# Kernel optimization log

Measured on AMD Instinct MI355X. Metric: run time of the kernel, lower is better.

## Reference

```python
import jax, jax.numpy as jnp
import numpy as np

BN_EPS = 1e-5
L2_EPS = 1e-12


def setup_inputs() -> dict:
    key = jax.random.key(0)
    k1, k2, k3 = jax.random.split(key, 3)
    B, N, D, K, G = 32, 2048, 512, 64, 16
    init_sc = 1.0 / np.sqrt(D)
    x = jax.random.normal(k1, (B, N, D), dtype=jnp.float32)
    clusters = init_sc * jax.random.normal(k2, (D, K + G), dtype=jnp.float32)
    clusters2 = init_sc * jax.random.normal(k3, (1, D, K), dtype=jnp.float32)
    bn_gamma = jnp.ones((K + G,), dtype=jnp.float32)
    bn_beta = jnp.zeros((K + G,), dtype=jnp.float32)
    return {"x": x, "clusters": clusters, "clusters2": clusters2,
            "bn_gamma": bn_gamma, "bn_beta": bn_beta}


def reference(x, clusters, clusters2, bn_gamma, bn_beta):
    B, N, D = x.shape
    K = clusters2.shape[-1]
    xf = x.reshape(B * N, D)
    # soft cluster assignment: [B*N, K+G]
    assn = xf @ clusters
    # BatchNorm1d (training-mode batch statistics, biased variance)
    mean = jnp.mean(assn, axis=0)
    var = jnp.var(assn, axis=0)
    assn = (assn - mean) * jax.lax.rsqrt(var + BN_EPS) * bn_gamma + bn_beta
    # softmax over clusters, then drop ghost clusters
    assn = jax.nn.softmax(assn, axis=1)[:, :K].reshape(B, N, K)
    # residual aggregation
    a_sum = jnp.sum(assn, axis=1, keepdims=True)          # [B, 1, K]
    a = a_sum * clusters2                                  # [B, D, K]
    vlad = jnp.einsum("bnk,bnd->bdk", assn, x) - a         # [B, D, K]
    # intra-normalization across feature dim D
    vlad = vlad / jnp.maximum(jnp.linalg.norm(vlad, axis=1, keepdims=True), L2_EPS)
    # flatten and global L2 normalization
    vlad = vlad.reshape(B, D * K)
    vlad = vlad / jnp.maximum(jnp.linalg.norm(vlad, axis=1, keepdims=True), L2_EPS)
    return vlad
```

## Files before the change

kernel.cpp:

```cpp
#include <hip/hip_runtime.h>
#include <hip/hip_bf16.h>
#include <stdint.h>

typedef __attribute__((ext_vector_type(8))) short short8;
typedef __attribute__((ext_vector_type(4))) float f32x4;

__device__ __forceinline__ float b2f(uint16_t u) {
  union { uint32_t i; float f; } v; v.i = ((uint32_t)u) << 16; return v.f;
}
__device__ __forceinline__ uint16_t f2b(float f) {
  uint32_t u = __float_as_uint(f);
  return (uint16_t)((u + 0x7FFFu + ((u >> 16) & 1u)) >> 16);
}
__device__ __forceinline__ uint32_t pk2(uint32_t lo, uint32_t hi) {
  return __builtin_amdgcn_perm(hi + 0x8000u, lo + 0x8000u, 0x07060302u);
}

__global__ void k0_prep(const float* __restrict__ clusters,
                        uint16_t* __restrict__ cB) {
  int gid = blockIdx.x * 256 + threadIdx.x;
  if (gid < 40960) {
    int i = gid & 7, chunk = gid >> 3;
    int lr = chunk & 15, q = (chunk >> 4) & 3, c5 = chunk >> 6;
    int n = c5 % 5, kk = c5 / 5;
    cB[gid] = f2b(clusters[(kk * 32 + q * 8 + i) * 80 + n * 16 + lr]);
  }
}

__global__ __launch_bounds__(256) void k1_gemm1(
    const float* __restrict__ x, const uint16_t* __restrict__ cB,
    float* __restrict__ raw, float* __restrict__ part) {
  __shared__ __align__(16) uint16_t lB[80 * 512];
  const int t = threadIdx.x;
  const int w = t >> 6, lane = t & 63, q = lane >> 4, lr = lane & 15;
  const int rbase = blockIdx.x * 128 + w * 32;

  {
    const uint4* src = (const uint4*)cB;
#pragma unroll 4
    for (int it = 0; it < 20; ++it)
      *(uint4*)&lB[(it * 256 + t) * 8] = src[it * 256 + t];
  }

  f32x4 acc[2][5];
#pragma unroll
  for (int m = 0; m < 2; ++m)
#pragma unroll
    for (int n = 0; n < 5; ++n) acc[m][n] = 0.f;

  const float* xa = x + (size_t)(rbase + lr) * 512 + q * 8;
  __syncthreads();

#pragma unroll 8
  for (int kk = 0; kk < 16; ++kk) {
    short8 a[2], bf[5];
#pragma unroll
    for (int m = 0; m < 2; ++m) {
      uint4 u0 = *(const uint4*)(xa + (size_t)m * 16 * 512 + kk * 32);
      uint4 u1 = *(const uint4*)(xa + (size_t)m * 16 * 512 + kk * 32 + 4);
      union { short8 s; uint32_t u[4]; } av;
      av.u[0] = pk2(u0.x, u0.y); av.u[1] = pk2(u0.z, u0.w);
      av.u[2] = pk2(u1.x, u1.y); av.u[3] = pk2(u1.z, u1.w);
      a[m] = av.s;
    }
#pragma unroll
    for (int n = 0; n < 5; ++n)
      bf[n] = *(const short8*)&lB[(((kk * 5 + n) * 4 + q) * 16 + lr) * 8];
#pragma unroll
    for (int m = 0; m < 2; ++m)
#pragma unroll
      for (int n = 0; n < 5; ++n)
        acc[m][n] = __builtin_amdgcn_mfma_f32_16x16x32_bf16(a[m], bf[n], acc[m][n], 0, 0, 0);
  }
  __syncthreads();

  float sums[5], sqs[5];
#pragma unroll
  for (int n = 0; n < 5; ++n) {
    float s = 0.f, qq = 0.f;
#pragma unroll
    for (int m = 0; m < 2; ++m) {
#pragma unroll
      for (int r = 0; r < 4; ++r) {
        float v = acc[m][n][r];
        s += v; qq += v * v;
        raw[(size_t)(rbase + m * 16 + q * 4 + r) * 80 + n * 16 + lr] = v;
      }
    }
    s += __shfl_xor(s, 16);  s += __shfl_xor(s, 32);
    qq += __shfl_xor(qq, 16); qq += __shfl_xor(qq, 32);
    sums[n] = s; sqs[n] = qq;
  }

  float* sf = (float*)lB;
  if (lane < 16) {
#pragma unroll
    for (int n = 0; n < 5; ++n) {
      sf[w * 160 + n * 16 + lr] = sums[n];
      sf[640 + w * 160 + n * 16 + lr] = sqs[n];
    }
  }
  __syncthreads();
  if (t < 160) {
    float a0 = sf[t] + sf[160 + t] + sf[320 + t] + sf[480 + t];
    float b0 = sf[640 + t] + sf[800 + t] + sf[960 + t] + sf[1120 + t];
    part[(size_t)t * 512 + blockIdx.x] = a0;
    part[(size_t)(160 + t) * 512 + blockIdx.x] = b0;
  }
}

__global__ __launch_bounds__(64) void k2_stats(
    const float* __restrict__ part, const float* __restrict__ gamma,
    const float* __restrict__ beta, float* __restrict__ scsh) {
  int c = blockIdx.x, t = threadIdx.x;
  const float* p1 = part + (size_t)c * 512;
  const float* p2 = part + (size_t)(160 + c) * 512;
  float s1 = 0.f, s2 = 0.f;
#pragma unroll
  for (int p = 0; p < 512; p += 64) { s1 += p1[p + t]; s2 += p2[p + t]; }
#pragma unroll
  for (int o = 1; o < 64; o <<= 1) { s1 += __shfl_xor(s1, o); s2 += __shfl_xor(s2, o); }
  if (t == 0) {
    float mean = s1 * (1.f / 65536.f);
    float var = s2 * (1.f / 65536.f) - mean * mean;
    float sc = rsqrtf(var + 1e-5f) * gamma[c];
    scsh[c] = sc;
    scsh[80 + c] = beta[c] - mean * sc;
  }
}

__global__ __launch_bounds__(256, 2) void k34_fused(
    const float* __restrict__ x, const float* __restrict__ raw_,
    const float* __restrict__ scsh, float* __restrict__ vpart,
    float* __restrict__ apart) {
  __shared__ __align__(16) uint16_t sx[2][256 * 40];
  __shared__ __align__(16) uint16_t sp[2][64 * 40];
  __shared__ float sc[80], sh[80];
  __shared__ float ared[4 * 64];

  const int t = threadIdx.x;
  const int b = blockIdx.x >> 4;
  const int s = (blockIdx.x >> 1) & 7;
  const int dh = blockIdx.x & 1;
  const int w = t >> 6, lane = t & 63, q = lane >> 4, lr = lane & 15;

  const int dd = t;
  const int sg = ((dd >> 2) + (dd >> 4)) & 3;
  const int r_ = t >> 3, cg = t & 7;
  const int kk_ = t & 63, ng = t >> 6;

  if (t < 80) sc[t] = scsh[t];
  else if (t < 160) sh[t - 80] = scsh[t];

  const float* xb = x + ((size_t)b * 2048 + (size_t)s * 256) * 512 + dh * 256;
  const float* rawb = raw_ + ((size_t)b * 2048 + (size_t)s * 256) * 80;

  f32x4 acc[4][4];
#pragma unroll
  for (int m = 0; m < 4; ++m)
#pragma unroll
    for (int j = 0; j < 4; ++j) acc[m][j] = 0.f;

  float xf[32], yf[10];
  float asum = 0.f;

#define XLOAD(c)                                                          \
  {                                                                       \
    const float* xc = xb + (size_t)(c) * 32 * 512 + dd;                   \
    _Pragma("unroll")                                                     \
    for (int j = 0; j < 32; ++j) xf[j] = xc[(size_t)j * 512];             \
  }
#define RLOAD(c)                                                          \
  {                                                                       \
    const float* rc = rawb + (size_t)((c) * 32 + r_) * 80 + cg * 10;      \
    _Pragma("unroll")                                                     \
    for (int j = 0; j < 5; ++j) {                                         \
      float2 v2 = *(const float2*)(rc + j * 2);                           \
      yf[2 * j] = v2.x; yf[2 * j + 1] = v2.y;                             \
    }                                                                     \
  }
#define XSTORE(buf)                                                       \
  {                                                                       \
    _Pragma("unroll")                                                     \
    for (int g = 0; g < 4; ++g) {                                         \
      union { uint4 u; uint32_t w4[4]; } pv;                              \
      _Pragma("unroll")                                                   \
      for (int h = 0; h < 4; ++h)                                         \
        pv.w4[h] = pk2(__float_as_uint(xf[g * 8 + h * 2]),                \
                       __float_as_uint(xf[g * 8 + h * 2 + 1]));           \
      *(uint4*)&sx[buf][dd * 40 + ((g ^ sg) << 3)] = pv.u;                \
    }                                                                     \
  }
#define SOFTMAX(buf)                                                      \
  {                                                                       \
    float yy[10]; float mx = -3.0e38f;                                    \
    _Pragma("unroll")                                                     \
    for (int j = 0; j < 10; ++j) {                                        \
      int cc = cg * 10 + j;                                               \
      yy[j] = yf[j] * sc[cc] + sh[cc];                                    \
      mx = fmaxf(mx, yy[j]);                                              \
    }                                                                     \
    mx = fmaxf(mx, __shfl_xor(mx, 1));                                    \
    mx = fmaxf(mx, __shfl_xor(mx, 2));                                    \
    mx = fmaxf(mx, __shfl_xor(mx, 4));                                    \
    float sum = 0.f;                                                      \
    _Pragma("unroll")                                                     \
    for (int j = 0; j < 10; ++j) { yy[j] = __expf(yy[j] - mx); sum += yy[j]; } \
    sum += __shfl_xor(sum, 1);                                            \
    sum += __shfl_xor(sum, 2);                                            \
    sum += __shfl_xor(sum, 4);                                            \
    float inv = 1.0f / sum;                                               \
    _Pragma("unroll")                                                     \
    for (int j = 0; j < 10; ++j) {                                        \
      int cc = cg * 10 + j;                                               \
      if (cc < 64) sp[buf][cc * 40 + r_] = f2b(yy[j] * inv);              \
    }                                                                     \
  }
#define GEMM(buf)                                                         \
  {                                                                       \
    const uint16_t* sxc = sx[buf];                                        \
    const uint16_t* spc = sp[buf];                                        \
    short8 bfr[4];                                                        \
    _Pragma("unroll")                                                     \
    for (int j = 0; j < 4; ++j)                                           \
      bfr[j] = *(const short8*)&spc[(j * 16 + lr) * 40 + (q << 3)];       \
    _Pragma("unroll")                                                     \
    for (int m = 0; m < 4; ++m) {                                         \
      int row = w * 64 + m * 16 + lr;                                     \
      int swr = ((row >> 2) + (row >> 4)) & 3;                            \
      short8 af = *(const short8*)&sxc[row * 40 + ((q ^ swr) << 3)];      \
      _Pragma("unroll")                                                   \
      for (int j = 0; j < 4; ++j)                                         \
        acc[m][j] = __builtin_amdgcn_mfma_f32_16x16x32_bf16(af, bfr[j], acc[m][j], 0, 0, 0); \
    }                                                                     \
    union { uint4 u; uint16_t us[8]; } pv;                                \
    pv.u = *(const uint4*)&spc[kk_ * 40 + (ng << 3)];                     \
    _Pragma("unroll")                                                     \
    for (int i = 0; i < 8; ++i) asum += b2f(pv.us[i]);                    \
  }

  XLOAD(0) RLOAD(0)
  __syncthreads();
  XSTORE(0) SOFTMAX(0)
  XLOAD(1) RLOAD(1)
  __syncthreads();

  for (int c = 0; c < 8; ++c) {
    const int cur = c & 1;
    GEMM(cur)
    __syncthreads();
    if (c < 7) {
      XSTORE(cur ^ 1) SOFTMAX(cur ^ 1)
      if (c < 6) { XLOAD(c + 2) RLOAD(c + 2) }
      __syncthreads();
    }
  }
#undef XLOAD
#undef RLOAD
#undef XSTORE
#undef SOFTMAX
#undef GEMM

  ared[ng * 64 + kk_] = asum;
  __syncthreads();
  if (dh == 0 && t < 64) {
    float a = ared[t] + ared[64 + t] + ared[128 + t] + ared[192 + t];
    apart[((size_t)b * 8 + s) * 64 + t] = a;
  }

  float* vp = vpart + ((size_t)s * 32 + b) * 32768;
#pragma unroll
  for (int m = 0; m < 4; ++m)
#pragma unroll
    for (int j = 0; j < 4; ++j)
#pragma unroll
      for (int r2 = 0; r2 < 4; ++r2)
        vp[(size_t)(dh * 256 + w * 64 + m * 16 + q * 4 + r2) * 64 + j * 16 + lr] =
            acc[m][j][r2];
}

__global__ __launch_bounds__(256) void k5a_red(
    const float* __restrict__ vpart, const float* __restrict__ apart,
    const float* __restrict__ c2, float* __restrict__ vfull,
    float* __restrict__ csq) {
  __shared__ float las[64];
  __shared__ float sred[256];
  const int t = threadIdx.x, b = blockIdx.x >> 4, dg = blockIdx.x & 15;
  if (t < 64) {
    float a = 0.f;
#pragma unroll
    for (int s = 0; s < 8; ++s) a += apart[((size_t)b * 8 + s) * 64 + t];
    las[t] = a;
  }
  __syncthreads();
  const int k = t & 63, di = t >> 6;
  float ssq = 0.f;
#pragma unroll
  for (int jj = 0; jj < 8; ++jj) {
    int d = dg * 32 + di * 8 + jj;
    size_t i = (size_t)d * 64 + k;
    float v = -las[k] * c2[i];
#pragma unroll
    for (int s = 0; s < 8; ++s) v += vpart[((size_t)s * 32 + b) * 32768 + i];
    vfull[(size_t)b * 32768 + i] = v;
    ssq += v * v;
  }
  sred[di * 64 + k] = ssq;
  __syncthreads();
  if (t < 64) {
    csq[(size_t)blockIdx.x * 64 + t] =
        sred[t] + sred[64 + t] + sred[128 + t] + sred[192 + t];
  }
}

__global__ __launch_bounds__(64) void k5b_fin(
    const float* __restrict__ csq, float* __restrict__ linv,
    float* __restrict__ gscl) {
  const int t = threadIdx.x, b = blockIdx.x;
  float ssq = 0.f;
#pragma unroll
  for (int dg = 0; dg < 16; ++dg) ssq += csq[(size_t)(b * 16 + dg) * 64 + t];
  float iv = 1.0f / fmaxf(sqrtf(ssq), 1e-12f);
  linv[b * 64 + t] = iv;
  float contrib = ssq * iv * iv;
#pragma unroll
  for (int o = 1; o < 64; o <<= 1) contrib += __shfl_xor(contrib, o);
  if (t == 0) gscl[b] = 1.0f / fmaxf(sqrtf(contrib), 1e-12f);
}

__global__ __launch_bounds__(256) void k5c_norm(
    const float* __restrict__ vfull, const float* __restrict__ linv,
    const float* __restrict__ gscl, float* __restrict__ out) {
  __shared__ float lv[64];
  __shared__ float gs;
  const int t = threadIdx.x, b = blockIdx.x >> 4, seg = blockIdx.x & 15;
  if (t < 64) lv[t] = linv[b * 64 + t];
  if (t == 64) gs = gscl[b];
  __syncthreads();
  const float gg = gs;
#pragma unroll
  for (int u = 0; u < 2; ++u) {
    int i = seg * 2048 + u * 1024 + t * 4;
    int k0 = i & 63;
    float4 a = *(const float4*)(vfull + (size_t)b * 32768 + i);
    float4 o;
    o.x = a.x * lv[k0 + 0] * gg;
    o.y = a.y * lv[k0 + 1] * gg;
    o.z = a.z * lv[k0 + 2] * gg;
    o.w = a.w * lv[k0 + 3] * gg;
    *(float4*)&out[(size_t)b * 32768 + i] = o;
  }
}

extern "C" void kernel_launch(void* const* d_in, const int* in_sizes, int n_in,
                              void* d_out, int out_size, void* d_ws, size_t ws_size,
                              hipStream_t stream) {
  const float* x         = (const float*)d_in[0];
  const float* clusters  = (const float*)d_in[1];
  const float* clusters2 = (const float*)d_in[2];
  const float* gamma     = (const float*)d_in[3];
  const float* beta      = (const float*)d_in[4];
  float* out = (float*)d_out;
  char* ws = (char*)d_ws;

  uint16_t* cB = (uint16_t*)(ws + 0);
  float* part  = (float*)(ws + 81920);
  float* scsh  = (float*)(ws + 737280);
  float* raw   = (float*)(ws + 737920);
  float* vpart = (float*)(ws + 21709440);
  float* vfull = (float*)(ws + 55263872);
  float* apart = (float*)(ws + 59458176);
  float* csq   = (float*)(ws + 59523712);
  float* linv  = (float*)(ws + 59654784);
  float* gscl  = (float*)(ws + 59662976);

  hipLaunchKernelGGL(k0_prep,   dim3(160), dim3(256), 0, stream, clusters, cB);
  hipLaunchKernelGGL(k1_gemm1,  dim3(512), dim3(256), 0, stream, x, cB, raw, part);
  hipLaunchKernelGGL(k2_stats,  dim3(80),  dim3(64),  0, stream, part, gamma, beta, scsh);
  hipLaunchKernelGGL(k34_fused, dim3(512), dim3(256), 0, stream, x, raw, scsh, vpart, apart);
  hipLaunchKernelGGL(k5a_red,   dim3(512), dim3(256), 0, stream, vpart, apart, clusters2, vfull, csq);
  hipLaunchKernelGGL(k5b_fin,   dim3(32),  dim3(64),  0, stream, csq, linv, gscl);
  hipLaunchKernelGGL(k5c_norm,  dim3(512), dim3(256), 0, stream, vfull, linv, gscl, out);
}
```

Baseline: 249.2 us.

## Read GEMM1 B operand from global, reorder VLAD loop barriers, vectorize reduction

Result: no change. 249.6 us (+0.2%).

```diff
diff --git a/kernel.cpp b/kernel.cpp
--- a/kernel.cpp
+++ b/kernel.cpp
@@ -30,18 +30,11 @@
 __global__ __launch_bounds__(256) void k1_gemm1(
     const float* __restrict__ x, const uint16_t* __restrict__ cB,
     float* __restrict__ raw, float* __restrict__ part) {
-  __shared__ __align__(16) uint16_t lB[80 * 512];
+  __shared__ float sf[1280];
   const int t = threadIdx.x;
   const int w = t >> 6, lane = t & 63, q = lane >> 4, lr = lane & 15;
   const int rbase = blockIdx.x * 128 + w * 32;
 
-  {
-    const uint4* src = (const uint4*)cB;
-#pragma unroll 4
-    for (int it = 0; it < 20; ++it)
-      *(uint4*)&lB[(it * 256 + t) * 8] = src[it * 256 + t];
-  }
-
   f32x4 acc[2][5];
 #pragma unroll
   for (int m = 0; m < 2; ++m)
@@ -49,9 +42,9 @@
     for (int n = 0; n < 5; ++n) acc[m][n] = 0.f;
 
   const float* xa = x + (size_t)(rbase + lr) * 512 + q * 8;
-  __syncthreads();
-
-#pragma unroll 8
+  const short8* cbq = (const short8*)cB + q * 16 + lr;
+
+#pragma unroll 2
   for (int kk = 0; kk < 16; ++kk) {
     short8 a[2], bf[5];
 #pragma unroll
@@ -65,14 +58,13 @@
     }
 #pragma unroll
     for (int n = 0; n < 5; ++n)
-      bf[n] = *(const short8*)&lB[(((kk * 5 + n) * 4 + q) * 16 + lr) * 8];
+      bf[n] = cbq[(kk * 5 + n) * 64];
 #pragma unroll
     for (int m = 0; m < 2; ++m)
 #pragma unroll
       for (int n = 0; n < 5; ++n)
         acc[m][n] = __builtin_amdgcn_mfma_f32_16x16x32_bf16(a[m], bf[n], acc[m][n], 0, 0, 0);
   }
-  __syncthreads();
 
   float sums[5], sqs[5];
 #pragma unroll
@@ -92,7 +84,6 @@
     sums[n] = s; sqs[n] = qq;
   }
 
-  float* sf = (float*)lB;
   if (lane < 16) {
 #pragma unroll
     for (int n = 0; n < 5; ++n) {
@@ -247,13 +238,12 @@
 
   for (int c = 0; c < 8; ++c) {
     const int cur = c & 1;
-    GEMM(cur)
-    __syncthreads();
     if (c < 7) {
       XSTORE(cur ^ 1) SOFTMAX(cur ^ 1)
       if (c < 6) { XLOAD(c + 2) RLOAD(c + 2) }
-      __syncthreads();
-    }
+    }
+    GEMM(cur)
+    __syncthreads();
   }
 #undef XLOAD
 #undef RLOAD
@@ -284,7 +274,7 @@
     const float* __restrict__ c2, float* __restrict__ vfull,
     float* __restrict__ csq) {
   __shared__ float las[64];
-  __shared__ float sred[256];
+  __shared__ float sred[16 * 64];
   const int t = threadIdx.x, b = blockIdx.x >> 4, dg = blockIdx.x & 15;
   if (t < 64) {
     float a = 0.f;
@@ -293,23 +283,33 @@
     las[t] = a;
   }
   __syncthreads();
-  const int k = t & 63, di = t >> 6;
-  float ssq = 0.f;
-#pragma unroll
-  for (int jj = 0; jj < 8; ++jj) {
-    int d = dg * 32 + di * 8 + jj;
-    size_t i = (size_t)d * 64 + k;
-    float v = -las[k] * c2[i];
-#pragma unroll
-    for (int s = 0; s < 8; ++s) v += vpart[((size_t)s * 32 + b) * 32768 + i];
-    vfull[(size_t)b * 32768 + i] = v;
-    ssq += v * v;
-  }
-  sred[di * 64 + k] = ssq;
+  const int di = t >> 4, kq = t & 15;
+  const float4 lasv = *(const float4*)&las[kq * 4];
+  float4 ssq = {0.f, 0.f, 0.f, 0.f};
+#pragma unroll
+  for (int jj = 0; jj < 2; ++jj) {
+    int d = dg * 32 + jj * 16 + di;
+    size_t i = (size_t)d * 64 + kq * 4;
+    float4 cc = *(const float4*)(c2 + i);
+    float4 v;
+    v.x = -lasv.x * cc.x; v.y = -lasv.y * cc.y;
+    v.z = -lasv.z * cc.z; v.w = -lasv.w * cc.w;
+#pragma unroll
+    for (int s = 0; s < 8; ++s) {
+      float4 p = *(const float4*)(vpart + ((size_t)s * 32 + b) * 32768 + i);
+      v.x += p.x; v.y += p.y; v.z += p.z; v.w += p.w;
+    }
+    *(float4*)(vfull + (size_t)b * 32768 + i) = v;
+    ssq.x += v.x * v.x; ssq.y += v.y * v.y;
+    ssq.z += v.z * v.z; ssq.w += v.w * v.w;
+  }
+  *(float4*)&sred[di * 64 + kq * 4] = ssq;
   __syncthreads();
   if (t < 64) {
-    csq[(size_t)blockIdx.x * 64 + t] =
-        sred[t] + sred[64 + t] + sred[128 + t] + sred[192 + t];
+    float s0 = 0.f;
+#pragma unroll
+    for (int di2 = 0; di2 < 16; ++di2) s0 += sred[di2 * 64 + t];
+    csq[(size_t)blockIdx.x * 64 + t] = s0;
   }
 }
 
```
